# Performance work log

Hardware: AMD Instinct MI355X
Metric: run time of the kernel (lower is better)

## Reference

```python
import jax, jax.numpy as jnp
import numpy as np

B, S, E, H, D = 4, 2048, 1024, 16, 64   # batch, seq, embed, heads, head_dim
NUM_BUCKETS, MAX_DISTANCE = 32, 128


def _relative_position_bucket(relative_position, num_buckets, max_distance):
    # causal T5-style bucketing
    max_exact = num_buckets // 2
    max_distance = max(max_distance, max_exact + 1)
    distance = jnp.maximum(-relative_position, 0)
    is_small = distance < max_exact
    safe_distance = jnp.maximum(distance, 1)
    log_scale = jnp.log(safe_distance / max_exact) / jnp.log(max_distance / max_exact)
    large_bucket = max_exact + (log_scale * (num_buckets - max_exact)).astype(jnp.int32)
    large_bucket = jnp.minimum(large_bucket, num_buckets - 1)
    return jnp.where(is_small, distance, large_bucket)


def setup_inputs() -> dict:
    key = jax.random.key(0)
    ks = jax.random.split(key, 7)
    w_scale = 1.0 / np.sqrt(E)
    inputs_q = jax.random.normal(ks[0], (B, S, E), jnp.float32)
    inputs_kv = jax.random.normal(ks[1], (B, S, E), jnp.float32)
    Wq = jax.random.normal(ks[2], (E, H * D), jnp.float32) * w_scale
    Wk = jax.random.normal(ks[3], (E, H * D), jnp.float32) * w_scale
    Wv = jax.random.normal(ks[4], (E, H * D), jnp.float32) * w_scale
    Wo = jax.random.normal(ks[5], (H * D, E), jnp.float32) * (1.0 / np.sqrt(H * D))
    rel_bias = jax.random.normal(ks[6], (H, NUM_BUCKETS), jnp.float32) * 0.02
    mask = jnp.tril(jnp.ones((S, S), dtype=bool))[None, None]  # [1,1,Q,K] causal
    return {"inputs_q": inputs_q, "inputs_kv": inputs_kv, "mask": mask,
            "Wq": Wq, "Wk": Wk, "Wv": Wv, "Wo": Wo, "rel_bias": rel_bias}


def reference(inputs_q, inputs_kv, mask, Wq, Wk, Wv, Wo, rel_bias):
    batch, q_len, embed = inputs_q.shape
    k_len = inputs_kv.shape[1]
    q = (inputs_q @ Wq).reshape(batch, q_len, H, D)
    k = (inputs_kv @ Wk).reshape(batch, k_len, H, D)
    v = (inputs_kv @ Wv).reshape(batch, k_len, H, D)
    attention = jnp.einsum("bqhd,bkhd->bhqk", q, k) * (1.0 / jnp.sqrt(D))
    # T5 relative position bias
    rel_pos = jnp.arange(k_len, dtype=jnp.int32)[None, :] - jnp.arange(q_len, dtype=jnp.int32)[:, None]
    bucket = _relative_position_bucket(rel_pos, NUM_BUCKETS, MAX_DISTANCE)  # [Q,K]
    attention = attention + jnp.take(rel_bias, bucket, axis=1)[None]  # [1,H,Q,K]
    attention = jnp.where(mask, attention, jnp.finfo(jnp.float32).min)
    normalized = jax.nn.softmax(attention, axis=-1)
    output = jnp.einsum("bhqk,bkhd->bqhd", normalized, v).reshape(batch, q_len, H * D)
    return output @ Wo
```

## Files before the change

kernel.cpp:

```cpp
#include <hip/hip_runtime.h>

typedef unsigned short u16;
typedef unsigned int u32;
typedef __bf16 bf16x8 __attribute__((ext_vector_type(8)));
typedef float f32x4 __attribute__((ext_vector_type(4)));
typedef float f32x16 __attribute__((ext_vector_type(16)));

#define S_LEN 2048
#define EMB 1024
#define NH 16
#define HD 64
#define LOG2E 1.44269504088896f

__device__ __forceinline__ u16 f2bf(float f) {
  union { float f; unsigned u; } v; v.f = f;
  unsigned r = (v.u + 0x7fffu + ((v.u >> 16) & 1u)) >> 16;
  return (u16)r;
}

__device__ __forceinline__ u32 packbf(float a, float b) {
  union { __bf16 h[2]; u32 u; } x;
  x.h[0] = (__bf16)a; x.h[1] = (__bf16)b;
  return x.u;
}

__device__ __forceinline__ void g2l16(const void* g, void* l) {
  __builtin_amdgcn_global_load_lds(
      (const unsigned int __attribute__((address_space(1)))*)g,
      (unsigned int __attribute__((address_space(3)))*)l, 16, 0, 0);
}


__global__ void cvt_bf16(const float* __restrict__ src, u16* __restrict__ dst, int n4) {
  int i = blockIdx.x * blockDim.x + threadIdx.x;
  if (i < n4) {
    float4 f = ((const float4*)src)[i];
    ushort4 o;
    o.x = f2bf(f.x); o.y = f2bf(f.y); o.z = f2bf(f.z); o.w = f2bf(f.w);
    ((ushort4*)dst)[i] = o;
  }
}

__global__ void transcvt(const float* __restrict__ W, u16* __restrict__ Wt) {
  __shared__ float t[32][33];
  int k0 = blockIdx.x * 32, n0 = blockIdx.y * 32;
  int tx = threadIdx.x & 31, ty = threadIdx.x >> 5;
#pragma unroll
  for (int i = 0; i < 4; i++) t[ty + i * 8][tx] = W[(k0 + ty + i * 8) * 1024 + n0 + tx];
  __syncthreads();
#pragma unroll
  for (int i = 0; i < 4; i++) Wt[(n0 + ty + i * 8) * 1024 + k0 + tx] = f2bf(t[tx][ty + i * 8]);
}

__global__ void build_bias(const float* __restrict__ rel, float* __restrict__ tbl) {
  int i = blockIdx.x * 256 + threadIdx.x;
  int h = i >> 11, dist = i & 2047;
  int bk;
  if (dist < 16) {
    bk = dist;
  } else {
    float ls = logf((float)dist * (1.0f / 16.0f)) * (1.0f / logf(8.0f));
    bk = 16 + (int)(ls * 16.0f);
    if (bk > 31) bk = 31;
  }
  tbl[i] = rel[h * 32 + bk];
}


template <int MODE>
__global__ __launch_bounds__(256, 2) void gemm_bf16(const u16* __restrict__ A,
                                                    const u16* __restrict__ Bt,
                                                    void* __restrict__ C, float scale) {
  constexpr int K = EMB;
  __shared__ u16 As[128 * 32];
  __shared__ u16 Bs[128 * 32];
  const int m0 = blockIdx.y * 128;
  const int n0 = blockIdx.x * 128;
  const int tid = threadIdx.x;
  const int lane = tid & 63;
  const int wid = tid >> 6;
  const int wm = (wid >> 1) * 64;
  const int wn = (wid & 1) * 64;
  const int la = lane & 15;
  const int lg = lane >> 4;

  const int r0 = tid >> 2;
  const int c0 = ((tid & 3) ^ (r0 & 3)) * 8;
  const u16* gA = A + (size_t)(m0 + r0) * K + c0;
  const u16* gB = Bt + (size_t)(n0 + r0) * K + c0;
  u16* lA = As + tid * 8;
  u16* lB = Bs + tid * 8;

  f32x4 acc[4][4] = {};

  for (int k0 = 0; k0 < K; k0 += 32) {
    g2l16(gA, lA);
    g2l16(gA + 64 * K, lA + 2048);
    g2l16(gB, lB);
    g2l16(gB + 64 * K, lB + 2048);
    gA += 32;
    gB += 32;
    __syncthreads();
    bf16x8 af[4], bb[4];
#pragma unroll
    for (int mf = 0; mf < 4; mf++) {
      int row = wm + mf * 16 + la;
      af[mf] = *(const bf16x8*)&As[row * 32 + ((lg ^ (row & 3)) << 3)];
    }
#pragma unroll
    for (int nf = 0; nf < 4; nf++) {
      int row = wn + nf * 16 + la;
      bb[nf] = *(const bf16x8*)&Bs[row * 32 + ((lg ^ (row & 3)) << 3)];
    }
#pragma unroll
    for (int mf = 0; mf < 4; mf++)
#pragma unroll
      for (int nf = 0; nf < 4; nf++)
        acc[mf][nf] =
            __builtin_amdgcn_mfma_f32_16x16x32_bf16(af[mf], bb[nf], acc[mf][nf], 0, 0, 0);
    __syncthreads();
  }

#pragma unroll
  for (int mf = 0; mf < 4; mf++)
#pragma unroll
    for (int nf = 0; nf < 4; nf++)
#pragma unroll
      for (int r = 0; r < 4; r++) {
        int m = m0 + wm + mf * 16 + lg * 4 + r;
        int n = n0 + wn + nf * 16 + la;
        float v = acc[mf][nf][r] * scale;
        if constexpr (MODE == 0) {
          int b = m >> 11, s = m & 2047, h = n >> 6, d = n & 63;
          ((u16*)C)[(((size_t)(b * 16 + h) * 2048 + s) << 6) + d] = f2bf(v);
        } else if constexpr (MODE == 1) {
          int b = m >> 11, s = m & 2047, h = n >> 6, d = n & 63;
          ((u16*)C)[(((size_t)(b * 16 + h) * 64 + d) << 11) + s] = f2bf(v);
        } else {
          ((float*)C)[(size_t)m * 1024 + n] = v;
        }
      }
}


__global__ __launch_bounds__(256, 2) void attn_kernel(const u16* __restrict__ Qb,
                                                      const u16* __restrict__ Kb,
                                                      const u16* __restrict__ Vtb,
                                                      const float* __restrict__ btbl,
                                                      u16* __restrict__ O) {
  __shared__ u16 Ks[64 * 64];
  __shared__ u16 Vs[64 * 64];
  __shared__ float bias_s[S_LEN];

  const int bh = blockIdx.x;
  const int h = bh & (NH - 1);
  const int b = bh >> 4;
  const int qt = 15 - blockIdx.y;
  const int q0 = qt * 128;
  const int tid = threadIdx.x;
  const int lane = tid & 63;
  const int w = tid >> 6;
  const int la = lane & 31;
  const int hi = lane >> 5;

  {
    const float4* src = (const float4*)(btbl + h * S_LEN);
    float4* dst = (float4*)bias_s;
    dst[tid] = src[tid];
    dst[tid + 256] = src[tid + 256];
  }

  const u16* Qg = Qb + (size_t)bh * S_LEN * HD;
  const u16* Kg = Kb + (size_t)bh * S_LEN * HD;
  const u16* Vg = Vtb + (size_t)bh * HD * S_LEN;

  const int qw = q0 + w * 32;
  const int q = qw + la;

  bf16x8 qfrag[4];
#pragma unroll
  for (int kk = 0; kk < 4; kk++)
    qfrag[kk] = *(const bf16x8*)&Qg[(size_t)q * HD + kk * 16 + hi * 8];

  f32x16 oacc[2] = {};
  float mrun = -1e30f;
  float lrun = 0.f;

  const int sr = tid >> 3;
  const int scz = ((tid & 7) ^ (sr & 7)) * 8;
  const u16* KgT = Kg + sr * 64 + scz;
  const u16* VgT = Vg + (size_t)sr * S_LEN + scz;
  u16* lK = Ks + tid * 8;
  u16* lV = Vs + tid * 8;

  const int nt = (q0 + 128) >> 6;
  const int qmax = qw + 31;

  for (int t = 0; t < nt; t++) {
    const int kv0 = t << 6;
    g2l16(KgT + kv0 * 64, lK);
    g2l16(KgT + kv0 * 64 + 32 * 64, lK + 2048);
    g2l16(VgT + kv0, lV);
    g2l16(VgT + kv0 + 32 * S_LEN, lV + 2048);
    __syncthreads();
    if (kv0 <= qmax) {
      f32x16 sacc[2] = {};
      __builtin_amdgcn_s_setprio(1);
#pragma unroll
      for (int kk = 0; kk < 4; kk++) {
#pragma unroll
        for (int nf = 0; nf < 2; nf++) {
          int row = nf * 32 + la;
          bf16x8 kf = *(const bf16x8*)&Ks[row * 64 + (((kk * 2 + hi) ^ (row & 7)) << 3)];
          sacc[nf] = __builtin_amdgcn_mfma_f32_32x32x16_bf16(kf, qfrag[kk], sacc[nf], 0, 0, 0);
        }
      }
      __builtin_amdgcn_s_setprio(0);

      float pf[32];
      const bool full = (kv0 + 63 <= qw);
#pragma unroll
      for (int nf = 0; nf < 2; nf++)
#pragma unroll
        for (int r = 0; r < 16; r++) {
          int kv = kv0 + nf * 32 + (r & 3) + ((r >> 2) << 3) + hi * 4;
          int bi = q - kv;
          if (bi < 0) bi = 0;
          float sb = sacc[nf][r] + bias_s[bi];
          if (!full) sb = (kv <= q) ? sb : -1e30f;
          pf[nf * 16 + r] = sb;
        }

      float tm[16];
#pragma unroll
      for (int i = 0; i < 16; i++) tm[i] = fmaxf(pf[i], pf[i + 16]);
#pragma unroll
      for (int i = 0; i < 8; i++) tm[i] = fmaxf(tm[i], tm[i + 8]);
#pragma unroll
      for (int i = 0; i < 4; i++) tm[i] = fmaxf(tm[i], tm[i + 4]);
      float mt = fmaxf(fmaxf(tm[0], tm[1]), fmaxf(tm[2], tm[3]));
      mt = fmaxf(mt, __shfl_xor(mt, 32));
      float mn = fmaxf(mrun, mt);
      float sc = exp2f((mrun - mn) * LOG2E);
      mrun = mn;
      float mnl = mn * LOG2E;
      float ts[16];
#pragma unroll
      for (int i = 0; i < 16; i++) {
        float p0 = exp2f(fmaf(pf[i], LOG2E, -mnl));
        float p1 = exp2f(fmaf(pf[i + 16], LOG2E, -mnl));
        pf[i] = p0;
        pf[i + 16] = p1;
        ts[i] = p0 + p1;
      }
#pragma unroll
      for (int i = 0; i < 8; i++) ts[i] += ts[i + 8];
#pragma unroll
      for (int i = 0; i < 4; i++) ts[i] += ts[i + 4];
      float rs = (ts[0] + ts[1]) + (ts[2] + ts[3]);
      rs += __shfl_xor(rs, 32);
      lrun = lrun * sc + rs;
#pragma unroll
      for (int d2 = 0; d2 < 2; d2++)
#pragma unroll
        for (int r = 0; r < 16; r++) oacc[d2][r] *= sc;

      u32 paw[4][4];
#pragma unroll
      for (int ks = 0; ks < 4; ks++) {
        const int nf = ks >> 1;
        const int e80 = (ks & 1) * 2;
#pragma unroll
        for (int half = 0; half < 2; half++) {
          u32 Y0 = packbf(pf[nf * 16 + 4 * e80 + 2 * half], pf[nf * 16 + 4 * e80 + 2 * half + 1]);
          u32 Y1 = packbf(pf[nf * 16 + 4 * (e80 + 1) + 2 * half],
                          pf[nf * 16 + 4 * (e80 + 1) + 2 * half + 1]);
          u32 Y0s = (u32)__shfl_xor((int)Y0, 32);
          u32 Y1s = (u32)__shfl_xor((int)Y1, 32);
          paw[ks][half] = hi ? Y1s : Y0;
          paw[ks][2 + half] = hi ? Y1 : Y0s;
        }
      }

      __builtin_amdgcn_s_setprio(1);
#pragma unroll
      for (int d2 = 0; d2 < 2; d2++) {
#pragma unroll
        for (int ks = 0; ks < 4; ks++) {
          int row = d2 * 32 + la;
          bf16x8 vf = *(const bf16x8*)&Vs[row * 64 + (((ks * 2 + hi) ^ (row & 7)) << 3)];
          union { u32 w[4]; bf16x8 v; } pu;
          pu.w[0] = paw[ks][0]; pu.w[1] = paw[ks][1];
          pu.w[2] = paw[ks][2]; pu.w[3] = paw[ks][3];
          oacc[d2] = __builtin_amdgcn_mfma_f32_32x32x16_bf16(vf, pu.v, oacc[d2], 0, 0, 0);
        }
      }
      __builtin_amdgcn_s_setprio(0);
    }
    __syncthreads();
  }

  const float inv = 1.0f / lrun;
  u16* Og = O + ((size_t)(b * S_LEN + q)) * EMB + h * HD;
#pragma unroll
  for (int d2 = 0; d2 < 2; d2++)
#pragma unroll
    for (int g = 0; g < 4; g++) {
      ushort4 ov;
      ov.x = f2bf(oacc[d2][g * 4 + 0] * inv);
      ov.y = f2bf(oacc[d2][g * 4 + 1] * inv);
      ov.z = f2bf(oacc[d2][g * 4 + 2] * inv);
      ov.w = f2bf(oacc[d2][g * 4 + 3] * inv);
      *(ushort4*)&Og[d2 * 32 + g * 8 + hi * 4] = ov;
    }
}


extern "C" void kernel_launch(void* const* d_in, const int* in_sizes, int n_in, void* d_out,
                              int out_size, void* d_ws, size_t ws_size, hipStream_t stream) {
  (void)in_sizes; (void)n_in; (void)out_size; (void)ws_size;
  const float* inq = (const float*)d_in[0];
  const float* inkv = (const float*)d_in[1];
  const float* Wq = (const float*)d_in[3];
  const float* Wk = (const float*)d_in[4];
  const float* Wv = (const float*)d_in[5];
  const float* Wo = (const float*)d_in[6];
  const float* rel = (const float*)d_in[7];
  float* out = (float*)d_out;

  char* ws = (char*)d_ws;
  size_t off = 0;
  auto alloc = [&](size_t bytes) {
    void* p = ws + off;
    off += (bytes + 255) & ~(size_t)255;
    return p;
  };
  u16* Aq = (u16*)alloc(16777216);
  u16* Akv = (u16*)alloc(16777216);
  u16* Wqt = (u16*)alloc(2097152);
  u16* Wkt = (u16*)alloc(2097152);
  u16* Wvt = (u16*)alloc(2097152);
  u16* Wot = (u16*)alloc(2097152);
  u16* Qb = (u16*)alloc(16777216);
  u16* Kb = (u16*)alloc(16777216);
  u16* Vtb = (u16*)alloc(16777216);
  u16* Ob = (u16*)alloc(16777216);
  float* btbl = (float*)alloc(131072);

  cvt_bf16<<<8192, 256, 0, stream>>>(inq, Aq, 2097152);
  cvt_bf16<<<8192, 256, 0, stream>>>(inkv, Akv, 2097152);
  transcvt<<<dim3(32, 32), 256, 0, stream>>>(Wq, Wqt);
  transcvt<<<dim3(32, 32), 256, 0, stream>>>(Wk, Wkt);
  transcvt<<<dim3(32, 32), 256, 0, stream>>>(Wv, Wvt);
  transcvt<<<dim3(32, 32), 256, 0, stream>>>(Wo, Wot);
  build_bias<<<128, 256, 0, stream>>>(rel, btbl);

  gemm_bf16<0><<<dim3(8, 64), 256, 0, stream>>>(Aq, Wqt, Qb, 0.125f);
  gemm_bf16<0><<<dim3(8, 64), 256, 0, stream>>>(Akv, Wkt, Kb, 1.0f);
  gemm_bf16<1><<<dim3(8, 64), 256, 0, stream>>>(Akv, Wvt, Vtb, 1.0f);
  attn_kernel<<<dim3(64, 16), 256, 0, stream>>>(Qb, Kb, Vtb, btbl, Ob);
  gemm_bf16<2><<<dim3(8, 64), 256, 0, stream>>>(Ob, Wot, out, 1.0f);
}
```

Before: 243.3 us.

## Double-buffer GEMM and attention tiles, lazy softmax rescale, permlane swaps

Adds LDS double buffering to both the projection GEMM and the attention kernel, issuing the next tile's global-to-LDS loads before computing on the current one and using explicit vmcnt waits with raw barriers. In the attention softmax it adds a far-region fast path that uses the constant bias, skips the online max rescale unless the max grows by more than a threshold, and replaces cross-half shuffles with permlane32_swap. These target global-load latency and softmax VALU/LDS shuffle overhead, at the cost of double the LDS per block, which may reduce occupancy. The lazy rescale also relies on exponent headroom for correctness.

```diff
diff --git a/kernel.cpp b/kernel.cpp
--- a/kernel.cpp
+++ b/kernel.cpp
@@ -28,6 +28,12 @@
   __builtin_amdgcn_global_load_lds(
       (const unsigned int __attribute__((address_space(1)))*)g,
       (unsigned int __attribute__((address_space(3)))*)l, 16, 0, 0);
+}
+
+__device__ __forceinline__ void permswap_f(float a, float b, float& x, float& y) {
+  auto r = __builtin_amdgcn_permlane32_swap(__float_as_int(a), __float_as_int(b), false, false);
+  x = __int_as_float(r[0]);
+  y = __int_as_float(r[1]);
 }
 
 
@@ -72,8 +78,8 @@
                                                     const u16* __restrict__ Bt,
                                                     void* __restrict__ C, float scale) {
   constexpr int K = EMB;
-  __shared__ u16 As[128 * 32];
-  __shared__ u16 Bs[128 * 32];
+  __shared__ u16 As[2][128 * 32];
+  __shared__ u16 Bs[2][128 * 32];
   const int m0 = blockIdx.y * 128;
   const int n0 = blockIdx.x * 128;
   const int tid = threadIdx.x;
@@ -88,29 +94,44 @@
   const int c0 = ((tid & 3) ^ (r0 & 3)) * 8;
   const u16* gA = A + (size_t)(m0 + r0) * K + c0;
   const u16* gB = Bt + (size_t)(n0 + r0) * K + c0;
-  u16* lA = As + tid * 8;
-  u16* lB = Bs + tid * 8;
 
   f32x4 acc[4][4] = {};
 
-  for (int k0 = 0; k0 < K; k0 += 32) {
-    g2l16(gA, lA);
-    g2l16(gA + 64 * K, lA + 2048);
-    g2l16(gB, lB);
-    g2l16(gB + 64 * K, lB + 2048);
-    gA += 32;
-    gB += 32;
-    __syncthreads();
+  g2l16(gA, As[0] + tid * 8);
+  g2l16(gA + 64 * K, As[0] + tid * 8 + 2048);
+  g2l16(gB, Bs[0] + tid * 8);
+  g2l16(gB + 64 * K, Bs[0] + tid * 8 + 2048);
+  gA += 32;
+  gB += 32;
+
+  for (int t = 0; t < 32; ++t) {
+    const int cur = t & 1;
+    if (t < 31) {
+      u16* lA = As[cur ^ 1] + tid * 8;
+      u16* lB = Bs[cur ^ 1] + tid * 8;
+      g2l16(gA, lA);
+      g2l16(gA + 64 * K, lA + 2048);
+      g2l16(gB, lB);
+      g2l16(gB + 64 * K, lB + 2048);
+      gA += 32;
+      gB += 32;
+      asm volatile("s_waitcnt vmcnt(4)" ::: "memory");
+    } else {
+      asm volatile("s_waitcnt vmcnt(0)" ::: "memory");
+    }
+    __builtin_amdgcn_s_barrier();
+    asm volatile("" ::: "memory");
+
     bf16x8 af[4], bb[4];
 #pragma unroll
     for (int mf = 0; mf < 4; mf++) {
       int row = wm + mf * 16 + la;
-      af[mf] = *(const bf16x8*)&As[row * 32 + ((lg ^ (row & 3)) << 3)];
+      af[mf] = *(const bf16x8*)&As[cur][row * 32 + ((lg ^ (row & 3)) << 3)];
     }
 #pragma unroll
     for (int nf = 0; nf < 4; nf++) {
       int row = wn + nf * 16 + la;
-      bb[nf] = *(const bf16x8*)&Bs[row * 32 + ((lg ^ (row & 3)) << 3)];
+      bb[nf] = *(const bf16x8*)&Bs[cur][row * 32 + ((lg ^ (row & 3)) << 3)];
     }
 #pragma unroll
     for (int mf = 0; mf < 4; mf++)
@@ -118,7 +139,10 @@
       for (int nf = 0; nf < 4; nf++)
         acc[mf][nf] =
             __builtin_amdgcn_mfma_f32_16x16x32_bf16(af[mf], bb[nf], acc[mf][nf], 0, 0, 0);
-    __syncthreads();
+
+    asm volatile("" ::: "memory");
+    __builtin_amdgcn_s_barrier();
+    asm volatile("" ::: "memory");
   }
 
 #pragma unroll
@@ -148,8 +172,8 @@
                                                       const u16* __restrict__ Vtb,
                                                       const float* __restrict__ btbl,
                                                       u16* __restrict__ O) {
-  __shared__ u16 Ks[64 * 64];
-  __shared__ u16 Vs[64 * 64];
+  __shared__ u16 Ks[2][64 * 64];
+  __shared__ u16 Vs[2][64 * 64];
   __shared__ float bias_s[S_LEN];
 
   const int bh = blockIdx.x;
@@ -188,21 +212,41 @@
 
   const int sr = tid >> 3;
   const int scz = ((tid & 7) ^ (sr & 7)) * 8;
-  const u16* KgT = Kg + sr * 64 + scz;
-  const u16* VgT = Vg + (size_t)sr * S_LEN + scz;
-  u16* lK = Ks + tid * 8;
-  u16* lV = Vs + tid * 8;
-
-  const int nt = (q0 + 128) >> 6;
+  const u16* kp = Kg + sr * 64 + scz;
+  const u16* vp = Vg + (size_t)sr * S_LEN + scz;
+
+  const int ntblk = (q0 + 128) >> 6;
   const int qmax = qw + 31;
 
-  for (int t = 0; t < nt; t++) {
+  g2l16(kp, Ks[0] + tid * 8);
+  g2l16(kp + 32 * 64, Ks[0] + tid * 8 + 2048);
+  g2l16(vp, Vs[0] + tid * 8);
+  g2l16(vp + 32 * S_LEN, Vs[0] + tid * 8 + 2048);
+  kp += 4096;
+  vp += 64;
+  __syncthreads();
+
+  const float bias31 = bias_s[S_LEN - 1];
+
+  for (int t = 0; t < ntblk; ++t) {
+    const int cur = t & 1;
+    if (t + 1 < ntblk) {
+      u16* lK = Ks[cur ^ 1] + tid * 8;
+      u16* lV = Vs[cur ^ 1] + tid * 8;
+      g2l16(kp, lK);
+      g2l16(kp + 32 * 64, lK + 2048);
+      g2l16(vp, lV);
+      g2l16(vp + 32 * S_LEN, lV + 2048);
+      kp += 4096;
+      vp += 64;
+      asm volatile("s_waitcnt vmcnt(4)" ::: "memory");
+    } else {
+      asm volatile("s_waitcnt vmcnt(0)" ::: "memory");
+    }
+    __builtin_amdgcn_s_barrier();
+    asm volatile("" ::: "memory");
+
     const int kv0 = t << 6;
-    g2l16(KgT + kv0 * 64, lK);
-    g2l16(KgT + kv0 * 64 + 32 * 64, lK + 2048);
-    g2l16(VgT + kv0, lV);
-    g2l16(VgT + kv0 + 32 * S_LEN, lV + 2048);
-    __syncthreads();
     if (kv0 <= qmax) {
       f32x16 sacc[2] = {};
       __builtin_amdgcn_s_setprio(1);
@@ -211,59 +255,88 @@
 #pragma unroll
         for (int nf = 0; nf < 2; nf++) {
           int row = nf * 32 + la;
-          bf16x8 kf = *(const bf16x8*)&Ks[row * 64 + (((kk * 2 + hi) ^ (row & 7)) << 3)];
+          bf16x8 kf = *(const bf16x8*)&Ks[cur][row * 64 + (((kk * 2 + hi) ^ (row & 7)) << 3)];
           sacc[nf] = __builtin_amdgcn_mfma_f32_32x32x16_bf16(kf, qfrag[kk], sacc[nf], 0, 0, 0);
         }
       }
       __builtin_amdgcn_s_setprio(0);
 
       float pf[32];
-      const bool full = (kv0 + 63 <= qw);
-#pragma unroll
-      for (int nf = 0; nf < 2; nf++)
-#pragma unroll
-        for (int r = 0; r < 16; r++) {
-          int kv = kv0 + nf * 32 + (r & 3) + ((r >> 2) << 3) + hi * 4;
-          int bi = q - kv;
-          if (bi < 0) bi = 0;
-          float sb = sacc[nf][r] + bias_s[bi];
-          if (!full) sb = (kv <= q) ? sb : -1e30f;
-          pf[nf * 16 + r] = sb;
+      float adde = 0.f;
+      if (kv0 + 176 <= qw) {
+#pragma unroll
+        for (int nf = 0; nf < 2; nf++)
+#pragma unroll
+          for (int r = 0; r < 16; r++) pf[nf * 16 + r] = sacc[nf][r];
+        adde = bias31;
+      } else {
+        const int qb2 = q - kv0 - 4 * hi;
+        const float* bp = bias_s + (qb2 - 59);
+        if (kv0 + 63 <= qw) {
+#pragma unroll
+          for (int nf = 0; nf < 2; nf++)
+#pragma unroll
+            for (int r = 0; r < 16; r++) {
+              const int Cn = nf * 32 + (r & 3) + ((r >> 2) << 3);
+              pf[nf * 16 + r] = sacc[nf][r] + bp[59 - Cn];
+            }
+        } else {
+#pragma unroll
+          for (int nf = 0; nf < 2; nf++)
+#pragma unroll
+            for (int r = 0; r < 16; r++) {
+              const int Cn = nf * 32 + (r & 3) + ((r >> 2) << 3);
+              pf[nf * 16 + r] = (Cn <= qb2) ? (sacc[nf][r] + bp[59 - Cn]) : -1e30f;
+            }
         }
-
-      float tm[16];
-#pragma unroll
-      for (int i = 0; i < 16; i++) tm[i] = fmaxf(pf[i], pf[i + 16]);
-#pragma unroll
-      for (int i = 0; i < 8; i++) tm[i] = fmaxf(tm[i], tm[i + 8]);
-#pragma unroll
-      for (int i = 0; i < 4; i++) tm[i] = fmaxf(tm[i], tm[i + 4]);
-      float mt = fmaxf(fmaxf(tm[0], tm[1]), fmaxf(tm[2], tm[3]));
-      mt = fmaxf(mt, __shfl_xor(mt, 32));
-      float mn = fmaxf(mrun, mt);
-      float sc = exp2f((mrun - mn) * LOG2E);
-      mrun = mn;
-      float mnl = mn * LOG2E;
-      float ts[16];
+      }
+
+      float a[11];
+#pragma unroll
+      for (int i = 0; i < 10; i++)
+        a[i] = fmaxf(fmaxf(pf[3 * i], pf[3 * i + 1]), pf[3 * i + 2]);
+      a[10] = fmaxf(pf[30], pf[31]);
+      float b0 = fmaxf(fmaxf(a[0], a[1]), a[2]);
+      float b1 = fmaxf(fmaxf(a[3], a[4]), a[5]);
+      float b2 = fmaxf(fmaxf(a[6], a[7]), a[8]);
+      float b3 = fmaxf(a[9], a[10]);
+      float mt = fmaxf(fmaxf(b0, b1), fmaxf(b2, b3)) + adde;
+      {
+        float x, y;
+        permswap_f(mt, mt, x, y);
+        mt = fmaxf(x, y);
+      }
+
+      if (__any(mt > mrun + 8.0f)) {
+        float mn = fmaxf(mrun, mt);
+        float sc = exp2f((mrun - mn) * LOG2E);
+        mrun = mn;
+        lrun *= sc;
+        oacc[0] *= sc;
+        oacc[1] *= sc;
+      }
+      const float ec = (adde - mrun) * LOG2E;
+
+      float ps[16];
 #pragma unroll
       for (int i = 0; i < 16; i++) {
-        float p0 = exp2f(fmaf(pf[i], LOG2E, -mnl));
-        float p1 = exp2f(fmaf(pf[i + 16], LOG2E, -mnl));
+        float p0 = exp2f(fmaf(pf[i], LOG2E, ec));
+        float p1 = exp2f(fmaf(pf[i + 16], LOG2E, ec));
         pf[i] = p0;
         pf[i + 16] = p1;
-        ts[i] = p0 + p1;
-      }
-#pragma unroll
-      for (int i = 0; i < 8; i++) ts[i] += ts[i + 8];
-#pragma unroll
-      for (int i = 0; i < 4; i++) ts[i] += ts[i + 4];
-      float rs = (ts[0] + ts[1]) + (ts[2] + ts[3]);
-      rs += __shfl_xor(rs, 32);
-      lrun = lrun * sc + rs;
-#pragma unroll
-      for (int d2 = 0; d2 < 2; d2++)
-#pragma unroll
-        for (int r = 0; r < 16; r++) oacc[d2][r] *= sc;
+        ps[i] = p0 + p1;
+      }
+#pragma unroll
+      for (int i = 0; i < 8; i++) ps[i] += ps[i + 8];
+#pragma unroll
+      for (int i = 0; i < 4; i++) ps[i] += ps[i + 4];
+      float rs = (ps[0] + ps[1]) + (ps[2] + ps[3]);
+      {
+        float x, y;
+        permswap_f(rs, rs, x, y);
+        rs = x + y;
+      }
+      lrun += rs;
 
       u32 paw[4][4];
 #pragma unroll
@@ -275,10 +348,9 @@
           u32 Y0 = packbf(pf[nf * 16 + 4 * e80 + 2 * half], pf[nf * 16 + 4 * e80 + 2 * half + 1]);
           u32 Y1 = packbf(pf[nf * 16 + 4 * (e80 + 1) + 2 * half],
                           pf[nf * 16 + 4 * (e80 + 1) + 2 * half + 1]);
-          u32 Y0s = (u32)__shfl_xor((int)Y0, 32);
-          u32 Y1s = (u32)__shfl_xor((int)Y1, 32);
-          paw[ks][half] = hi ? Y1s : Y0;
-          paw[ks][2 + half] = hi ? Y1 : Y0s;
+          auto r = __builtin_amdgcn_permlane32_swap((int)Y0, (int)Y1, false, false);
+          paw[ks][half] = (u32)r[0];
+          paw[ks][2 + half] = (u32)r[1];
         }
       }
 
@@ -288,7 +360,7 @@
 #pragma unroll
         for (int ks = 0; ks < 4; ks++) {
           int row = d2 * 32 + la;
-          bf16x8 vf = *(const bf16x8*)&Vs[row * 64 + (((ks * 2 + hi) ^ (row & 7)) << 3)];
+          bf16x8 vf = *(const bf16x8*)&Vs[cur][row * 64 + (((ks * 2 + hi) ^ (row & 7)) << 3)];
           union { u32 w[4]; bf16x8 v; } pu;
           pu.w[0] = paw[ks][0]; pu.w[1] = paw[ks][1];
           pu.w[2] = paw[ks][2]; pu.w[3] = paw[ks][3];
@@ -297,7 +369,10 @@
       }
       __builtin_amdgcn_s_setprio(0);
     }
-    __syncthreads();
+
+    asm volatile("" ::: "memory");
+    __builtin_amdgcn_s_barrier();
+    asm volatile("" ::: "memory");
   }
 
   const float inv = 1.0f / lrun;
```

Result: faster. 225.8 us (-7.2%).
